# Performance work log

Hardware: AMD Instinct MI355X
Metric: run time of the kernel (lower is better)

The kernel has to match this reference:

```python
import jax, jax.numpy as jnp
import numpy as np

N_HEADS = 16
ROPE_BASE = 10000.0


def _rope_cos_sin(seq_len, head_dim, dtype):
    half = head_dim // 2
    inv_freq = 1.0 / (ROPE_BASE ** (jnp.arange(0, half, dtype=jnp.float32) / half))
    ang = jnp.arange(seq_len, dtype=jnp.float32)[:, None] * inv_freq[None, :]  # [S, half]
    cos = jnp.concatenate([jnp.cos(ang), jnp.cos(ang)], axis=-1).astype(dtype)  # [S, hd]
    sin = jnp.concatenate([jnp.sin(ang), jnp.sin(ang)], axis=-1).astype(dtype)
    return cos, sin


def _rotate_half(x):
    half = x.shape[-1] // 2
    return jnp.concatenate([-x[..., half:], x[..., :half]], axis=-1)


def setup_inputs() -> dict:
    key = jax.random.key(0)
    k1, k2, k3 = jax.random.split(key, 3)
    B, S, D = 2, 2048, 1024
    x = jax.random.normal(k1, (B, S, D), dtype=jnp.float32)
    w_qkv = jax.random.normal(k2, (D, 3 * D), dtype=jnp.float32) * (1.0 / np.sqrt(D))
    w_out = jax.random.normal(k3, (D, D), dtype=jnp.float32) * (1.0 / np.sqrt(D))
    return {"x": x, "w_qkv": w_qkv, "w_out": w_out}


def reference(x, w_qkv, w_out):
    B, S, D = x.shape
    H = N_HEADS
    hd = D // H
    scale = 1.0 / np.sqrt(hd)

    qkv = x @ w_qkv  # [B, S, 3D]
    q, k, v = jnp.split(qkv, 3, axis=-1)
    # [B, H, S, hd]
    q = q.reshape(B, S, H, hd).transpose(0, 2, 1, 3)
    k = k.reshape(B, S, H, hd).transpose(0, 2, 1, 3)
    v = v.reshape(B, S, H, hd).transpose(0, 2, 1, 3)

    cos, sin = _rope_cos_sin(S, hd, x.dtype)  # [S, hd]
    q = q * cos + _rotate_half(q) * sin
    k = k * cos + _rotate_half(k) * sin

    scores = jnp.einsum("bhqd,bhkd->bhqk", q, k) * scale  # [B, H, S, S]
    causal = jnp.tril(jnp.ones((S, S), dtype=bool))
    scores = jnp.where(causal[None, None, :, :], scores, -jnp.inf)

    probs = jax.nn.softmax(scores.astype(jnp.float32), axis=-1).astype(q.dtype)
    out = jnp.einsum("bhqk,bhkd->bhqd", probs, v)  # [B, H, S, hd]
    out = out.transpose(0, 2, 1, 3).reshape(B, S, D)
    return out @ w_out
```

## Files before the change

### kernel.cpp

```cpp
#include <hip/hip_runtime.h>
#include <math.h>
#include <type_traits>

#define B_  2
#define S_  2048
#define D_  1024
#define H_  16

typedef short bf16x8 __attribute__((ext_vector_type(8)));
typedef short bf16x4 __attribute__((ext_vector_type(4)));
typedef float f32x4  __attribute__((ext_vector_type(4)));

__device__ __forceinline__ short f2bf(float f) {
    unsigned u = __builtin_bit_cast(unsigned, f);
    u += 0x7FFFu + ((u >> 16) & 1u);
    return (short)(u >> 16);
}
__device__ __forceinline__ float bf2f(short s) {
    unsigned u = ((unsigned)(unsigned short)s) << 16;
    return __builtin_bit_cast(float, u);
}

__device__ __forceinline__ void gload16(const short* g, const void* l) {
    __builtin_amdgcn_global_load_lds(
        (const __attribute__((address_space(1))) void*)g,
        (__attribute__((address_space(3))) void*)l, 16, 0, 0);
}

__global__ __launch_bounds__(256) void cvt_bf16_kernel(
    const float* __restrict__ in, short* __restrict__ out)
{
    int i = (blockIdx.x * 256 + threadIdx.x) * 8;
    float4 a = *(const float4*)(in + i);
    float4 b = *(const float4*)(in + i + 4);
    bf16x8 o;
    o[0] = f2bf(a.x); o[1] = f2bf(a.y); o[2] = f2bf(a.z); o[3] = f2bf(a.w);
    o[4] = f2bf(b.x); o[5] = f2bf(b.y); o[6] = f2bf(b.z); o[7] = f2bf(b.w);
    *(bf16x8*)(out + i) = o;
}

__global__ __launch_bounds__(256) void transpose_cvt_kernel(
    const float* __restrict__ in, short* __restrict__ out, int K, int N)
{
    __shared__ short t[64][72];
    const int k0 = blockIdx.y * 64, n0 = blockIdx.x * 64;
    const int r = threadIdx.x >> 2;
    const int c = (threadIdx.x & 3) * 16;
    const float* src = in + (size_t)(k0 + r) * N + n0 + c;
#pragma unroll
    for (int i = 0; i < 16; ++i) t[c + i][r] = f2bf(src[i]);
    __syncthreads();
    short* dst = out + (size_t)(n0 + r) * K + k0 + c;
    *(bf16x8*)(dst)     = *(const bf16x8*)&t[r][c];
    *(bf16x8*)(dst + 8) = *(const bf16x8*)&t[r][c + 8];
}

__global__ __launch_bounds__(256) void rope_tab_kernel(float2* __restrict__ tab)
{
    int idx = blockIdx.x * 256 + threadIdx.x;
    int j = idx & 31, s = idx >> 5;
    float inv = powf(10000.0f, -(float)j * (1.0f / 32.0f));
    float sn, cs;
    sincosf((float)s * inv, &sn, &cs);
    tab[idx] = make_float2(cs, sn);
}

__global__ __launch_bounds__(256) void gemm_bt_f32(
    const short* __restrict__ A, const short* __restrict__ Bt,
    float* __restrict__ C, int M, int N, int K)
{
    __shared__ short smem[18432];

    const int tid  = threadIdx.x;
    const int wave = tid >> 6, lane = tid & 63;
    const int quad = lane >> 4, l16 = lane & 15;
    const int wm = wave >> 1, wn = wave & 1;
    const int row0 = blockIdx.y * 128, col0 = blockIdx.x * 64;

    f32x4 acc[4][2];
#pragma unroll
    for (int mi = 0; mi < 4; ++mi)
#pragma unroll
        for (int ni = 0; ni < 2; ++ni) acc[mi][ni] = (f32x4)0.f;

    const int sr = tid >> 2;
    const int sc = (tid & 3) * 8;
    const short* a0 = A  + (size_t)(row0 + sr) * K + sc;
    const short* a1 = A  + (size_t)(row0 + 64 + sr) * K + sc;
    const short* b0 = Bt + (size_t)(col0 + sr) * K + sc;

    auto stage = [&](int b, int kt) {
        char* l = (char*)(smem + b * 6144) + wave * 1024;
        const int k0 = kt * 32;
        gload16(a0 + k0, l);
        gload16(a1 + k0, l + 4096);
        gload16(b0 + k0, l + 8192);
    };

    const int NT = K >> 5;
    stage(0, 0);
    stage(1, 1);
    int bufid = 0;
    for (int kt = 0; kt < NT; ++kt) {
        if (kt + 1 < NT) { asm volatile("s_waitcnt vmcnt(3)" ::: "memory"); }
        else             { asm volatile("s_waitcnt vmcnt(0)" ::: "memory"); }
        __builtin_amdgcn_s_barrier();
        __builtin_amdgcn_sched_barrier(0);
        if (kt + 2 < NT) {
            int nb = bufid + 2; if (nb >= 3) nb -= 3;
            stage(nb, kt + 2);
        }

        const short* As = smem + bufid * 6144;
        const short* Bs = As + 4096;
        bf16x8 af[4], bfr[2];
#pragma unroll
        for (int mi = 0; mi < 4; ++mi)
            af[mi] = *(const bf16x8*)(As + (wm * 64 + mi * 16 + l16) * 32 + quad * 8);
#pragma unroll
        for (int ni = 0; ni < 2; ++ni)
            bfr[ni] = *(const bf16x8*)(Bs + (wn * 32 + ni * 16 + l16) * 32 + quad * 8);
#pragma unroll
        for (int mi = 0; mi < 4; ++mi)
#pragma unroll
            for (int ni = 0; ni < 2; ++ni)
                acc[mi][ni] = __builtin_amdgcn_mfma_f32_16x16x32_bf16(
                    af[mi], bfr[ni], acc[mi][ni], 0, 0, 0);

        bufid = (bufid + 1 == 3) ? 0 : bufid + 1;
    }

#pragma unroll
    for (int mi = 0; mi < 4; ++mi)
#pragma unroll
        for (int ni = 0; ni < 2; ++ni)
#pragma unroll
            for (int r = 0; r < 4; ++r) {
                int row = row0 + wm * 64 + mi * 16 + quad * 4 + r;
                int col = col0 + wn * 32 + ni * 16 + l16;
                C[(size_t)row * N + col] = acc[mi][ni][r];
            }
}

__global__ __launch_bounds__(256) void gemm_qkv(
    const short* __restrict__ A, const short* __restrict__ Bt,
    const float2* __restrict__ tab,
    short* __restrict__ Qb, short* __restrict__ Kb, short* __restrict__ Vt)
{
    const int K = 1024;
    extern __shared__ short smem[];
    short* Sc = smem;

    const int tid  = threadIdx.x;
    const int wave = tid >> 6, lane = tid & 63;
    const int quad = lane >> 4, l16 = lane & 15;
    const int wm = wave >> 1, wn = wave & 1;
    const int row0 = blockIdx.y * 128, col0 = blockIdx.x * 128;

    f32x4 acc[4][4];
#pragma unroll
    for (int mi = 0; mi < 4; ++mi)
#pragma unroll
        for (int ni = 0; ni < 4; ++ni) acc[mi][ni] = (f32x4)0.f;

    const int sr = tid >> 2;
    const int sc = (tid & 3) * 8;
    const short* a0 = A  + (size_t)(row0 + sr) * K + sc;
    const short* a1 = A  + (size_t)(row0 + 64 + sr) * K + sc;
    const short* b0 = Bt + (size_t)(col0 + sr) * K + sc;
    const short* b1 = Bt + (size_t)(col0 + 64 + sr) * K + sc;

    auto stage = [&](int b, int kt) {
        char* l = (char*)(smem + b * 8192) + wave * 1024;
        const int k0 = kt * 32;
        gload16(a0 + k0, l);
        gload16(a1 + k0, l + 4096);
        gload16(b0 + k0, l + 8192);
        gload16(b1 + k0, l + 12288);
    };

    const int NT = K >> 5;
    stage(0, 0);
    stage(1, 1);
    int bufid = 0;
    for (int kt = 0; kt < NT; ++kt) {
        if (kt + 1 < NT) { asm volatile("s_waitcnt vmcnt(4)" ::: "memory"); }
        else             { asm volatile("s_waitcnt vmcnt(0)" ::: "memory"); }
        __builtin_amdgcn_s_barrier();
        __builtin_amdgcn_sched_barrier(0);
        if (kt + 2 < NT) {
            int nb = bufid + 2; if (nb >= 3) nb -= 3;
            stage(nb, kt + 2);
        }

        const short* As = smem + bufid * 8192;
        const short* Bs = As + 4096;
        bf16x8 af[4], bfr[4];
#pragma unroll
        for (int mi = 0; mi < 4; ++mi)
            af[mi] = *(const bf16x8*)(As + (wm * 64 + mi * 16 + l16) * 32 + quad * 8);
#pragma unroll
        for (int ni = 0; ni < 4; ++ni)
            bfr[ni] = *(const bf16x8*)(Bs + (wn * 64 + ni * 16 + l16) * 32 + quad * 8);
#pragma unroll
        for (int mi = 0; mi < 4; ++mi)
#pragma unroll
            for (int ni = 0; ni < 4; ++ni)
                acc[mi][ni] = __builtin_amdgcn_mfma_f32_16x16x32_bf16(
                    af[mi], bfr[ni], acc[mi][ni], 0, 0, 0);

        bufid = (bufid + 1 == 3) ? 0 : bufid + 1;
    }

    __syncthreads();

    const int sec  = (col0 + wn * 64) >> 6;
    const int h    = sec & 15;
    const int kind = sec >> 4;
    short* myS = Sc + wave * 4608;

    const int mrow0 = row0 + wm * 64;
    const int b  = mrow0 >> 11;
    const int bh = b * 16 + h;
    const int sbase = mrow0 & (S_ - 1);

    if (kind < 2) {
#pragma unroll
        for (int mi = 0; mi < 4; ++mi) {
#pragma unroll
            for (int r = 0; r < 4; ++r) {
                int sl = mi * 16 + quad * 4 + r;
                int s = sbase + sl;
#pragma unroll
                for (int ni = 0; ni < 2; ++ni) {
                    int j = ni * 16 + l16;
                    float2 t = tab[s * 32 + j];
                    float lo = acc[mi][ni][r], hi = acc[mi][ni + 2][r];
                    float olo = lo * t.x - hi * t.y;
                    float ohi = hi * t.x + lo * t.y;
                    if (kind == 0) { olo *= 0.125f; ohi *= 0.125f; }
                    myS[sl * 72 + j]      = f2bf(olo);
                    myS[sl * 72 + 32 + j] = f2bf(ohi);
                }
            }
        }
        const int rl = lane >> 3;
        const int cl = (lane & 7) * 8;
        if (kind == 0) {
#pragma unroll
            for (int p = 0; p < 8; ++p) {
                int rr = p * 8 + rl;
                bf16x8 v = *(const bf16x8*)&myS[rr * 72 + cl];
                *(bf16x8*)(Qb + ((size_t)bh * S_ + sbase + rr) * 64 + cl) = v;
            }
        } else {
#pragma unroll
            for (int p = 0; p < 8; ++p) {
                int rr = p * 8 + rl;
                bf16x8 v = *(const bf16x8*)&myS[rr * 72 + cl];
                *(bf16x8*)(Kb + ((size_t)bh * S_ + sbase + rr) * 72 + cl) = v;
            }
        }
    } else {
#pragma unroll
        for (int mi = 0; mi < 4; ++mi)
#pragma unroll
            for (int ni = 0; ni < 4; ++ni) {
                bf16x4 p;
                p[0] = f2bf(acc[mi][ni][0]);
                p[1] = f2bf(acc[mi][ni][1]);
                p[2] = f2bf(acc[mi][ni][2]);
                p[3] = f2bf(acc[mi][ni][3]);
                *(bf16x4*)&myS[(ni * 16 + l16) * 72 + mi * 16 + quad * 4] = p;
            }
        const int rl = lane >> 3;
        const int cl = (lane & 7) * 8;
#pragma unroll
        for (int p = 0; p < 8; ++p) {
            int dd = p * 8 + rl;
            bf16x8 v = *(const bf16x8*)&myS[dd * 72 + cl];
            *(bf16x8*)(Vt + ((size_t)bh * 64 + dd) * S_ + sbase + cl) = v;
        }
    }
}

__global__ __launch_bounds__(256) void attn_kernel(
    const short* __restrict__ Qb, const short* __restrict__ Kb,
    const short* __restrict__ Vt, short* __restrict__ Opart,
    float* __restrict__ lpart)
{
    __shared__ short Ks[2][64 * 72];
    __shared__ short Vs[2][64 * 72];
    __shared__ short Ps[64][72];

    const int lin = blockIdx.x;
    const int xcd = lin & 7;
    const int j   = lin >> 3;
    const int bh   = xcd * 4 + (j & 3);
    const int task = j >> 2;

    const int g = task < 8 ? 0 : task < 24 ? 1 : task < 48 ? 2 : 3;
    const int cumstart = g == 0 ? 0 : g == 1 ? 8 : g == 2 ? 24 : 48;
    const int idx = task - cumstart;
    const int qd = idx / (g + 1);
    const int qb = 8 * g + qd;
    const int c  = idx - qd * (g + 1);
    const int t0 = c * 8;
    const int t1 = min(qb, c * 8 + 7);

    const int wave = threadIdx.x >> 6, lane = threadIdx.x & 63;
    const int quad = lane >> 4, l16 = lane & 15;
    const size_t head64 = (size_t)bh * S_ * 64;
    const size_t headK  = (size_t)bh * S_ * 72;

    const short* qrow = Qb + head64
        + (size_t)(qb * 64 + wave * 16 + l16) * 64 + quad * 8;
    const bf16x8 qf0 = *(const bf16x8*)(qrow);
    const bf16x8 qf1 = *(const bf16x8*)(qrow + 32);

    bf16x8 ones;
#pragma unroll
    for (int i = 0; i < 8; ++i) ones[i] = (short)0x3F80;

    int vr[3], vc[3];
#pragma unroll
    for (int u = 0; u < 3; ++u) {
        int jj = wave + u * 4;
        int e = jj * 64 + lane;
        vr[u] = e / 9;
        vc[u] = e * 8 - vr[u] * 72;
    }

    auto stageKV = [&](int buf, int t) {
        const short* kt  = Kb + headK + (size_t)t * 4608;
        const short* vtb = Vt + head64 + t * 64;
        short* kl = Ks[buf];
        short* vl = Vs[buf];
#pragma unroll
        for (int u = 0; u < 3; ++u) {
            int jj = wave + u * 4;
            if (jj < 9) {
                gload16(kt + jj * 512 + lane * 8, (char*)kl + jj * 1024);
                gload16(vtb + (size_t)vr[u] * S_ + vc[u], (char*)vl + jj * 1024);
            }
        }
    };

    f32x4 lacc = (f32x4)0.f;
    f32x4 oacc[4];
#pragma unroll
    for (int nt = 0; nt < 4; ++nt) oacc[nt] = (f32x4)0.f;

    int buf = 0;
    stageKV(0, t0);
    for (int t = t0; t <= t1; ++t) {
        __syncthreads();
        if (t < t1) stageKV(buf ^ 1, t + 1);

        const short* kb = Ks[buf];
        const short* vb = Vs[buf];

        f32x4 s4[4];
#pragma unroll
        for (int nt = 0; nt < 4; ++nt) {
            const short* kr = kb + (nt * 16 + l16) * 72 + quad * 8;
            bf16x8 b0 = *(const bf16x8*)kr;
            bf16x8 b1 = *(const bf16x8*)(kr + 32);
            f32x4 a = (f32x4)0.f;
            a = __builtin_amdgcn_mfma_f32_16x16x32_bf16(qf0, b0, a, 0, 0, 0);
            a = __builtin_amdgcn_mfma_f32_16x16x32_bf16(qf1, b1, a, 0, 0, 0);
            s4[nt] = a;
        }

        if (t == qb) {
#pragma unroll
            for (int nt = 0; nt < 4; ++nt)
#pragma unroll
                for (int r = 0; r < 4; ++r)
                    if (nt * 16 + l16 > wave * 16 + quad * 4 + r)
                        s4[nt][r] = -INFINITY;
        }

#pragma unroll
        for (int nt = 0; nt < 4; ++nt)
#pragma unroll
            for (int r = 0; r < 4; ++r)
                Ps[wave * 16 + quad * 4 + r][nt * 16 + l16] =
                    f2bf(__expf(s4[nt][r] - 8.0f));

        bf16x8 pa0 = *(const bf16x8*)&Ps[wave * 16 + l16][quad * 8];
        bf16x8 pa1 = *(const bf16x8*)&Ps[wave * 16 + l16][32 + quad * 8];
        lacc = __builtin_amdgcn_mfma_f32_16x16x32_bf16(pa0, ones, lacc, 0, 0, 0);
        lacc = __builtin_amdgcn_mfma_f32_16x16x32_bf16(pa1, ones, lacc, 0, 0, 0);
#pragma unroll
        for (int nt = 0; nt < 4; ++nt) {
            const short* vrp = vb + (nt * 16 + l16) * 72 + quad * 8;
            bf16x8 vb0 = *(const bf16x8*)vrp;
            bf16x8 vb1 = *(const bf16x8*)(vrp + 32);
            oacc[nt] = __builtin_amdgcn_mfma_f32_16x16x32_bf16(
                pa0, vb0, oacc[nt], 0, 0, 0);
            oacc[nt] = __builtin_amdgcn_mfma_f32_16x16x32_bf16(
                pa1, vb1, oacc[nt], 0, 0, 0);
        }
        buf ^= 1;
    }

    const int pidx = bh * 80 + task;
#pragma unroll
    for (int r = 0; r < 4; ++r) {
        int ql = wave * 16 + quad * 4 + r;
        short* orow = Opart + (size_t)pidx * 4096 + ql * 64;
#pragma unroll
        for (int nt = 0; nt < 4; ++nt)
            orow[nt * 16 + l16] = f2bf(oacc[nt][r]);
        if (l16 == 0)
            lpart[(size_t)pidx * 64 + ql] = lacc[r];
    }
}

__global__ __launch_bounds__(256) void combine_kernel(
    const short* __restrict__ Opart, const float* __restrict__ lpart,
    short* __restrict__ attnb)
{
    const int qb = blockIdx.x, bh = blockIdx.y;
    const int g = qb >> 3, nch = g + 1;
    const int cbase = bh * 80 + nch * (qb - 4 * g);
    const int q = threadIdx.x >> 2;
    const int dg = (threadIdx.x & 3) * 16;

    float lsum = 0.f;
    float acc[16];
#pragma unroll
    for (int i = 0; i < 16; ++i) acc[i] = 0.f;

    for (int cc = 0; cc < nch; ++cc) {
        lsum += lpart[(size_t)(cbase + cc) * 64 + q];
        const short* src = Opart + (size_t)(cbase + cc) * 4096 + q * 64 + dg;
        bf16x8 o0 = *(const bf16x8*)src;
        bf16x8 o1 = *(const bf16x8*)(src + 8);
#pragma unroll
        for (int i = 0; i < 8; ++i) {
            acc[i]     += bf2f(o0[i]);
            acc[i + 8] += bf2f(o1[i]);
        }
    }
    float inv = 1.0f / lsum;
    const int b = bh >> 4, h = bh & 15;
    bf16x8 r0, r1;
#pragma unroll
    for (int i = 0; i < 8; ++i) {
        r0[i] = f2bf(acc[i] * inv);
        r1[i] = f2bf(acc[i + 8] * inv);
    }
    short* dst = attnb + (size_t)(b * S_ + qb * 64 + q) * 1024 + h * 64 + dg;
    *(bf16x8*)dst       = r0;
    *(bf16x8*)(dst + 8) = r1;
}

extern "C" void kernel_launch(void* const* d_in, const int* in_sizes, int n_in,
                              void* d_out, int out_size, void* d_ws, size_t ws_size,
                              hipStream_t stream)
{
    const float* x     = (const float*)d_in[0];
    const float* w_qkv = (const float*)d_in[1];
    const float* w_out = (const float*)d_in[2];
    float* out = (float*)d_out;

    short* Qb   = (short*)d_ws;
    short* Kb   = Qb   + (size_t)4096 * 1024;
    short* Vt   = Kb   + (size_t)32 * 2048 * 72;
    short* Xb   = Vt   + (size_t)4096 * 1024;
    short* Wqt  = Xb   + (size_t)4096 * 1024;
    short* Wot  = Wqt  + (size_t)3072 * 1024;
    float2* tab = (float2*)(Wot + (size_t)1024 * 1024);
    short* Opart = (short*)(tab + 2048 * 32);
    float* lbuf  = (float*)(Opart + (size_t)2560 * 4096);
    short* attnb = Xb;

    cvt_bf16_kernel<<<(4096 * 1024 / 8) / 256, 256, 0, stream>>>(x, Xb);
    transpose_cvt_kernel<<<dim3(3072 / 64, 1024 / 64), 256, 0, stream>>>(
        w_qkv, Wqt, 1024, 3072);
    transpose_cvt_kernel<<<dim3(1024 / 64, 1024 / 64), 256, 0, stream>>>(
        w_out, Wot, 1024, 1024);
    rope_tab_kernel<<<(2048 * 32) / 256, 256, 0, stream>>>(tab);

    gemm_qkv<<<dim3(3072 / 128, 4096 / 128), 256, 49152, stream>>>(
        Xb, Wqt, tab, Qb, Kb, Vt);

    attn_kernel<<<2560, 256, 0, stream>>>(Qb, Kb, Vt, Opart, lbuf);

    combine_kernel<<<dim3(32, 32), 256, 0, stream>>>(Opart, lbuf, attnb);

    gemm_bt_f32<<<dim3(1024 / 64, 4096 / 128), 256, 0, stream>>>(
        attnb, Wot, out, 4096, 1024, 1024);
}
```

Baseline: 187.0 us.

## Drop LDS K/V staging in attention; read K/V directly, two row tiles per wave

Attention blocks shrink from four waves to two, with each wave now covering 32 query rows. K and V are read straight from global memory instead of being double-buffered in LDS through async loads, which removes the per-tile __syncthreads. The S tile is computed transposed (K as the A operand) so P can be written to LDS as vector stores. K loses its padded 72-column layout and uses 64 columns to match. This trades shared staging and block-wide synchronisation for redundant global and L2 loads of K/V by each wave, and for higher register pressure.

```diff
diff --git a/kernel.cpp b/kernel.cpp
--- a/kernel.cpp
+++ b/kernel.cpp
@@ -246,20 +246,12 @@
         }
         const int rl = lane >> 3;
         const int cl = (lane & 7) * 8;
-        if (kind == 0) {
-#pragma unroll
-            for (int p = 0; p < 8; ++p) {
-                int rr = p * 8 + rl;
-                bf16x8 v = *(const bf16x8*)&myS[rr * 72 + cl];
-                *(bf16x8*)(Qb + ((size_t)bh * S_ + sbase + rr) * 64 + cl) = v;
-            }
-        } else {
-#pragma unroll
-            for (int p = 0; p < 8; ++p) {
-                int rr = p * 8 + rl;
-                bf16x8 v = *(const bf16x8*)&myS[rr * 72 + cl];
-                *(bf16x8*)(Kb + ((size_t)bh * S_ + sbase + rr) * 72 + cl) = v;
-            }
+        short* dst = (kind == 0 ? Qb : Kb);
+#pragma unroll
+        for (int p = 0; p < 8; ++p) {
+            int rr = p * 8 + rl;
+            bf16x8 v = *(const bf16x8*)&myS[rr * 72 + cl];
+            *(bf16x8*)(dst + ((size_t)bh * S_ + sbase + rr) * 64 + cl) = v;
         }
     } else {
 #pragma unroll
@@ -284,13 +276,11 @@
     }
 }
 
-__global__ __launch_bounds__(256) void attn_kernel(
+__global__ __launch_bounds__(128, 4) void attn_kernel(
     const short* __restrict__ Qb, const short* __restrict__ Kb,
     const short* __restrict__ Vt, short* __restrict__ Opart,
     float* __restrict__ lpart)
 {
-    __shared__ short Ks[2][64 * 72];
-    __shared__ short Vs[2][64 * 72];
     __shared__ short Ps[64][72];
 
     const int lin = blockIdx.x;
@@ -311,111 +301,109 @@
     const int wave = threadIdx.x >> 6, lane = threadIdx.x & 63;
     const int quad = lane >> 4, l16 = lane & 15;
     const size_t head64 = (size_t)bh * S_ * 64;
-    const size_t headK  = (size_t)bh * S_ * 72;
-
-    const short* qrow = Qb + head64
-        + (size_t)(qb * 64 + wave * 16 + l16) * 64 + quad * 8;
-    const bf16x8 qf0 = *(const bf16x8*)(qrow);
-    const bf16x8 qf1 = *(const bf16x8*)(qrow + 32);
+
+    bf16x8 qf[2][2];
+#pragma unroll
+    for (int m = 0; m < 2; ++m) {
+        const short* qrow = Qb + head64
+            + (size_t)(qb * 64 + wave * 32 + m * 16 + l16) * 64 + quad * 8;
+        qf[m][0] = *(const bf16x8*)(qrow);
+        qf[m][1] = *(const bf16x8*)(qrow + 32);
+    }
 
     bf16x8 ones;
 #pragma unroll
     for (int i = 0; i < 8; ++i) ones[i] = (short)0x3F80;
 
-    int vr[3], vc[3];
-#pragma unroll
-    for (int u = 0; u < 3; ++u) {
-        int jj = wave + u * 4;
-        int e = jj * 64 + lane;
-        vr[u] = e / 9;
-        vc[u] = e * 8 - vr[u] * 72;
-    }
-
-    auto stageKV = [&](int buf, int t) {
-        const short* kt  = Kb + headK + (size_t)t * 4608;
-        const short* vtb = Vt + head64 + t * 64;
-        short* kl = Ks[buf];
-        short* vl = Vs[buf];
-#pragma unroll
-        for (int u = 0; u < 3; ++u) {
-            int jj = wave + u * 4;
-            if (jj < 9) {
-                gload16(kt + jj * 512 + lane * 8, (char*)kl + jj * 1024);
-                gload16(vtb + (size_t)vr[u] * S_ + vc[u], (char*)vl + jj * 1024);
-            }
-        }
-    };
-
-    f32x4 lacc = (f32x4)0.f;
-    f32x4 oacc[4];
-#pragma unroll
-    for (int nt = 0; nt < 4; ++nt) oacc[nt] = (f32x4)0.f;
-
-    int buf = 0;
-    stageKV(0, t0);
+    f32x4 lacc[2] = {(f32x4)0.f, (f32x4)0.f};
+    f32x4 oacc[2][4];
+#pragma unroll
+    for (int m = 0; m < 2; ++m)
+#pragma unroll
+        for (int nt = 0; nt < 4; ++nt) oacc[m][nt] = (f32x4)0.f;
+
     for (int t = t0; t <= t1; ++t) {
-        __syncthreads();
-        if (t < t1) stageKV(buf ^ 1, t + 1);
-
-        const short* kb = Ks[buf];
-        const short* vb = Vs[buf];
-
-        f32x4 s4[4];
+        const short* kb = Kb + head64 + (size_t)t * 64 * 64;
+        const short* vb = Vt + head64 + t * 64;
+
+        f32x4 s4[2][4];
 #pragma unroll
         for (int nt = 0; nt < 4; ++nt) {
-            const short* kr = kb + (nt * 16 + l16) * 72 + quad * 8;
-            bf16x8 b0 = *(const bf16x8*)kr;
-            bf16x8 b1 = *(const bf16x8*)(kr + 32);
-            f32x4 a = (f32x4)0.f;
-            a = __builtin_amdgcn_mfma_f32_16x16x32_bf16(qf0, b0, a, 0, 0, 0);
-            a = __builtin_amdgcn_mfma_f32_16x16x32_bf16(qf1, b1, a, 0, 0, 0);
-            s4[nt] = a;
+            const short* kr = kb + (nt * 16 + l16) * 64 + quad * 8;
+            bf16x8 k0 = *(const bf16x8*)kr;
+            bf16x8 k1 = *(const bf16x8*)(kr + 32);
+#pragma unroll
+            for (int m = 0; m < 2; ++m) {
+                f32x4 a = (f32x4)0.f;
+                a = __builtin_amdgcn_mfma_f32_16x16x32_bf16(k0, qf[m][0], a, 0, 0, 0);
+                a = __builtin_amdgcn_mfma_f32_16x16x32_bf16(k1, qf[m][1], a, 0, 0, 0);
+                s4[m][nt] = a;
+            }
         }
 
         if (t == qb) {
 #pragma unroll
-            for (int nt = 0; nt < 4; ++nt)
+            for (int m = 0; m < 2; ++m)
+#pragma unroll
+                for (int nt = 0; nt < 4; ++nt)
+#pragma unroll
+                    for (int r = 0; r < 4; ++r)
+                        if (nt * 16 + quad * 4 + r > wave * 32 + m * 16 + l16)
+                            s4[m][nt][r] = -INFINITY;
+        }
+
+#pragma unroll
+        for (int m = 0; m < 2; ++m)
+#pragma unroll
+            for (int nt = 0; nt < 4; ++nt) {
+                bf16x4 p;
 #pragma unroll
                 for (int r = 0; r < 4; ++r)
-                    if (nt * 16 + l16 > wave * 16 + quad * 4 + r)
-                        s4[nt][r] = -INFINITY;
-        }
-
-#pragma unroll
-        for (int nt = 0; nt < 4; ++nt)
-#pragma unroll
-            for (int r = 0; r < 4; ++r)
-                Ps[wave * 16 + quad * 4 + r][nt * 16 + l16] =
-                    f2bf(__expf(s4[nt][r] - 8.0f));
-
-        bf16x8 pa0 = *(const bf16x8*)&Ps[wave * 16 + l16][quad * 8];
-        bf16x8 pa1 = *(const bf16x8*)&Ps[wave * 16 + l16][32 + quad * 8];
-        lacc = __builtin_amdgcn_mfma_f32_16x16x32_bf16(pa0, ones, lacc, 0, 0, 0);
-        lacc = __builtin_amdgcn_mfma_f32_16x16x32_bf16(pa1, ones, lacc, 0, 0, 0);
+                    p[r] = f2bf(__expf(s4[m][nt][r] - 8.0f));
+                *(bf16x4*)&Ps[wave * 32 + m * 16 + l16][nt * 16 + quad * 4] = p;
+            }
+
+        bf16x8 pa[2][2];
+#pragma unroll
+        for (int m = 0; m < 2; ++m) {
+            pa[m][0] = *(const bf16x8*)&Ps[wave * 32 + m * 16 + l16][quad * 8];
+            pa[m][1] = *(const bf16x8*)&Ps[wave * 32 + m * 16 + l16][32 + quad * 8];
+        }
+
+#pragma unroll
+        for (int m = 0; m < 2; ++m) {
+            lacc[m] = __builtin_amdgcn_mfma_f32_16x16x32_bf16(pa[m][0], ones, lacc[m], 0, 0, 0);
+            lacc[m] = __builtin_amdgcn_mfma_f32_16x16x32_bf16(pa[m][1], ones, lacc[m], 0, 0, 0);
+        }
+
 #pragma unroll
         for (int nt = 0; nt < 4; ++nt) {
-            const short* vrp = vb + (nt * 16 + l16) * 72 + quad * 8;
+            const short* vrp = vb + (size_t)(nt * 16 + l16) * S_ + quad * 8;
             bf16x8 vb0 = *(const bf16x8*)vrp;
             bf16x8 vb1 = *(const bf16x8*)(vrp + 32);
-            oacc[nt] = __builtin_amdgcn_mfma_f32_16x16x32_bf16(
-                pa0, vb0, oacc[nt], 0, 0, 0);
-            oacc[nt] = __builtin_amdgcn_mfma_f32_16x16x32_bf16(
-                pa1, vb1, oacc[nt], 0, 0, 0);
-        }
-        buf ^= 1;
+#pragma unroll
+            for (int m = 0; m < 2; ++m) {
+                oacc[m][nt] = __builtin_amdgcn_mfma_f32_16x16x32_bf16(
+                    pa[m][0], vb0, oacc[m][nt], 0, 0, 0);
+                oacc[m][nt] = __builtin_amdgcn_mfma_f32_16x16x32_bf16(
+                    pa[m][1], vb1, oacc[m][nt], 0, 0, 0);
+            }
+        }
     }
 
     const int pidx = bh * 80 + task;
 #pragma unroll
-    for (int r = 0; r < 4; ++r) {
-        int ql = wave * 16 + quad * 4 + r;
-        short* orow = Opart + (size_t)pidx * 4096 + ql * 64;
-#pragma unroll
-        for (int nt = 0; nt < 4; ++nt)
-            orow[nt * 16 + l16] = f2bf(oacc[nt][r]);
-        if (l16 == 0)
-            lpart[(size_t)pidx * 64 + ql] = lacc[r];
-    }
+    for (int m = 0; m < 2; ++m)
+#pragma unroll
+        for (int r = 0; r < 4; ++r) {
+            int ql = wave * 32 + m * 16 + quad * 4 + r;
+            short* orow = Opart + (size_t)pidx * 4096 + ql * 64;
+#pragma unroll
+            for (int nt = 0; nt < 4; ++nt)
+                orow[nt * 16 + l16] = f2bf(oacc[m][nt][r]);
+            if (l16 == 0)
+                lpart[(size_t)pidx * 64 + ql] = lacc[m][r];
+        }
 }
 
 __global__ __launch_bounds__(256) void combine_kernel(
@@ -468,7 +456,7 @@
 
     short* Qb   = (short*)d_ws;
     short* Kb   = Qb   + (size_t)4096 * 1024;
-    short* Vt   = Kb   + (size_t)32 * 2048 * 72;
+    short* Vt   = Kb   + (size_t)4096 * 1024;
     short* Xb   = Vt   + (size_t)4096 * 1024;
     short* Wqt  = Xb   + (size_t)4096 * 1024;
     short* Wot  = Wqt  + (size_t)3072 * 1024;
@@ -487,7 +475,7 @@
     gemm_qkv<<<dim3(3072 / 128, 4096 / 128), 256, 49152, stream>>>(
         Xb, Wqt, tab, Qb, Kb, Vt);
 
-    attn_kernel<<<2560, 256, 0, stream>>>(Qb, Kb, Vt, Opart, lbuf);
+    attn_kernel<<<2560, 128, 0, stream>>>(Qb, Kb, Vt, Opart, lbuf);
 
     combine_kernel<<<dim3(32, 32), 256, 0, stream>>>(Opart, lbuf, attnb);
 
```

Result: slower. 216.4 us (+15.7%).
